# Performance work log

Measured on AMD Instinct MI355X. Metric: run time of the kernel, lower is better.

The kernel has to match this reference:

```python
import jax, jax.numpy as jnp
import numpy as np

N_NODES = 100000
N_EDGES = 1000000
D = 64


def _sage_conv(x_src, x_self, src, dst, W_self, W_neigh, b, n_nodes):
    # mean aggregation over in-neighbors: gather src feats, segment-sum into dst
    gathered = x_src[src]                                            # [E, D]
    summed = jax.ops.segment_sum(gathered, dst, num_segments=n_nodes)  # [N, D]
    deg = jax.ops.segment_sum(jnp.ones_like(dst, dtype=x_src.dtype), dst,
                              num_segments=n_nodes)                  # [N]
    mean = summed / jnp.maximum(deg, 1.0)[:, None]  # zero-degree -> 0 (DGL semantics)
    # DGL SAGEConv: fc_self (with bias) + fc_neigh (no bias)
    return x_self @ W_self + b + mean @ W_neigh


def setup_inputs() -> dict:
    key = jax.random.key(0)
    ks = jax.random.split(key, 8)
    s = 1.0 / np.sqrt(D)
    return {
        "x": jax.random.normal(ks[0], (N_NODES, D), dtype=jnp.float32),
        "src": jax.random.randint(ks[1], (N_EDGES,), 0, N_NODES, dtype=jnp.int32),
        "dst": jax.random.randint(ks[2], (N_EDGES,), 0, N_NODES, dtype=jnp.int32),
        "W_self1": jax.random.normal(ks[3], (D, D), dtype=jnp.float32) * s,
        "W_neigh1": jax.random.normal(ks[4], (D, D), dtype=jnp.float32) * s,
        "b1": jnp.zeros((D,), dtype=jnp.float32),
        "W_self2": jax.random.normal(ks[5], (D, D), dtype=jnp.float32) * s,
        "W_neigh2": jax.random.normal(ks[6], (D, D), dtype=jnp.float32) * s,
        "b2": jnp.zeros((D,), dtype=jnp.float32),
    }


def reference(x, src, dst, W_self1, W_neigh1, b1, W_self2, W_neigh2, b2):
    n = x.shape[0]
    h = _sage_conv(x, x, src, dst, W_self1, W_neigh1, b1, n)
    h = jax.nn.relu(h)
    out = _sage_conv(h, h, src, dst, W_self2, W_neigh2, b2, n)
    return out
```

## Files before the change

### kernel.cpp

```cpp
#include <hip/hip_runtime.h>

#define DFEAT 64
typedef unsigned short bf16_t;

typedef __bf16 bf16x8 __attribute__((ext_vector_type(8)));
typedef float f32x4 __attribute__((ext_vector_type(4)));

#define NPB_SHIFT 7
#define NPB 128
#define BCAP 2048
#define ESLICE 2048
#define MEAN_STRIDE 72

__device__ __forceinline__ float bflo(unsigned int u) {
    union { unsigned int i; float f; } v;
    v.i = u << 16;
    return v.f;
}
__device__ __forceinline__ float bfhi(unsigned int u) {
    union { unsigned int i; float f; } v;
    v.i = u & 0xFFFF0000u;
    return v.f;
}
__device__ __forceinline__ unsigned short f2bf(float f) {
    unsigned int u = __float_as_uint(f);
    u += 0x7FFFu + ((u >> 16) & 1u);
    return (unsigned short)(u >> 16);
}

__global__ __launch_bounds__(256) void prep_all(const int* __restrict__ src,
                                                const int* __restrict__ dst,
                                                int* __restrict__ gcur,
                                                int* __restrict__ packbuf,
                                                int n_edges, int nbuck,
                                                const float* __restrict__ x,
                                                bf16_t* __restrict__ xb,
                                                bf16_t* __restrict__ hb, int n_half,
                                                const float* __restrict__ Ws1,
                                                const float* __restrict__ Wn1,
                                                const float* __restrict__ Ws2,
                                                const float* __restrict__ Wn2,
                                                bf16_t* __restrict__ wf1,
                                                bf16_t* __restrict__ wf2,
                                                int ab, int cb, int n_nodes) {
    const int tid = threadIdx.x;
    const int blk = blockIdx.x;
    if (blk < ab) {
        __shared__ int bhist[1024];
        __shared__ int bcur[1024];
        const long ebase = (long)blk * ESLICE;
        for (int i = tid; i < 1024; i += 256) bhist[i] = 0;
        __syncthreads();
        for (int i = 0; i < ESLICE / 256; ++i) {
            long e = ebase + i * 256 + tid;
            if (e < n_edges) atomicAdd(&bhist[dst[e] >> NPB_SHIFT], 1);
        }
        __syncthreads();
        for (int bb = tid; bb < nbuck; bb += 256) {
            int h = bhist[bb];
            bcur[bb] = h ? atomicAdd(&gcur[bb], h) : 0;
        }
        __syncthreads();
        for (int i = 0; i < ESLICE / 256; ++i) {
            long e = ebase + i * 256 + tid;
            if (e < n_edges) {
                int d = dst[e];
                int bb = d >> NPB_SHIFT;
                int slot = atomicAdd(&bcur[bb], 1);
                if (slot < BCAP)
                    packbuf[(size_t)bb * BCAP + slot] = ((d & (NPB - 1)) << 17) | src[e];
            }
        }
    } else if (blk < ab + cb) {
        int t = (blk - ab) * 256 + tid;
        if (t < n_half) {
            float2 v = ((const float2*)x)[t];
            ushort2 o;
            o.x = f2bf(v.x);
            o.y = f2bf(v.y);
            ((ushort2*)xb)[t] = o;
        }
    } else {
        for (int i = tid; i < 16 * 64 * 8; i += 256) {
            int j = i & 7;
            int l = (i >> 3) & 63;
            int f = i >> 9;
            int kk = f >> 2, nt = f & 3;
            int k = kk * 32 + (l >> 4) * 8 + j;
            int col = nt * 16 + (l & 15);
            float v1 = (k < 64) ? Ws1[k * 64 + col] : Wn1[(k - 64) * 64 + col];
            float v2 = (k < 64) ? Ws2[k * 64 + col] : Wn2[(k - 64) * 64 + col];
            wf1[i] = f2bf(v1);
            wf2[i] = f2bf(v2);
        }
        if (tid < DFEAT) {
            xb[(size_t)n_nodes * DFEAT + tid] = 0;
            hb[(size_t)n_nodes * DFEAT + tid] = 0;
        }
    }
}

__global__ __launch_bounds__(256) void fused_layer(const bf16_t* __restrict__ featb,
                                                   const int* __restrict__ gcur,
                                                   const int* __restrict__ packbuf,
                                                   const bf16_t* __restrict__ wf,
                                                   const float* __restrict__ bias,
                                                   float* __restrict__ outf,
                                                   bf16_t* __restrict__ outb,
                                                   int n_nodes, int do_relu, int zrow) {
    __shared__ int    elist[BCAP];
    __shared__ bf16_t meanL[NPB * MEAN_STRIDE];
    __shared__ int    hist[NPB];
    __shared__ int    scanb[NPB];
    __shared__ int    curL[NPB];

    const int tid = threadIdx.x;
    const int b   = blockIdx.x;

    if (tid < NPB) hist[tid] = 0;
    __syncthreads();

    const int count = min(gcur[b], BCAP);
    const int* pb = packbuf + (size_t)b * BCAP;

    int pkreg[BCAP / 256];
#pragma unroll
    for (int k = 0; k < BCAP / 256; ++k) {
        int i = tid + k * 256;
        if (i < count) {
            int pk = pb[i];
            pkreg[k] = pk;
            atomicAdd(&hist[(pk >> 17) & (NPB - 1)], 1);
        }
    }
    __syncthreads();

    int hv = (tid < NPB) ? hist[tid] : 0;
    int cp = (hv + 3) & ~3;
    if (tid < NPB) scanb[tid] = cp;
    __syncthreads();
    for (int off = 1; off < NPB; off <<= 1) {
        int t = 0;
        if (tid < NPB && tid >= off) t = scanb[tid - off];
        __syncthreads();
        if (tid < NPB) scanb[tid] += t;
        __syncthreads();
    }
    if (tid < NPB) {
        int ex = scanb[tid] - cp;
        scanb[tid] = ex;
        curL[tid]  = ex;
    }
    __syncthreads();

#pragma unroll
    for (int k = 0; k < BCAP / 256; ++k) {
        int i = tid + k * 256;
        if (i < count) {
            int pk = pkreg[k];
            int dl = (pk >> 17) & (NPB - 1);
            int pos = atomicAdd(&curL[dl], 1);
            if (pos < BCAP) elist[pos] = pk & 0x1FFFF;
        }
    }
    __syncthreads();
    if (tid < NPB) {
        int s0 = scanb[tid];
        int c  = hist[tid];
        int ce = s0 + ((c + 3) & ~3);
        for (int p = s0 + c; p < ce && p < BCAP; ++p) elist[p] = zrow;
    }
    __syncthreads();

    const int oct = tid >> 3;
    const int lo  = tid & 7;
#pragma unroll
    for (int n = 0; n < 4; ++n) {
        int r  = oct * 4 + n;
        int s0 = scanb[r];
        int c  = hist[r];
        int cpd = (c + 3) & ~3;
        float s0f = 0.f, s1f = 0.f, s2f = 0.f, s3f = 0.f;
        float s4f = 0.f, s5f = 0.f, s6f = 0.f, s7f = 0.f;
        int i = 0;
        for (; i + 8 <= cpd; i += 8) {
            int4 ea = *(const int4*)(elist + s0 + i);
            int4 eb = *(const int4*)(elist + s0 + i + 4);
            uint4 u0 = *(const uint4*)(featb + (size_t)ea.x * DFEAT + lo * 8);
            uint4 u1 = *(const uint4*)(featb + (size_t)ea.y * DFEAT + lo * 8);
            uint4 u2 = *(const uint4*)(featb + (size_t)ea.z * DFEAT + lo * 8);
            uint4 u3 = *(const uint4*)(featb + (size_t)ea.w * DFEAT + lo * 8);
            uint4 u4 = *(const uint4*)(featb + (size_t)eb.x * DFEAT + lo * 8);
            uint4 u5 = *(const uint4*)(featb + (size_t)eb.y * DFEAT + lo * 8);
            uint4 u6 = *(const uint4*)(featb + (size_t)eb.z * DFEAT + lo * 8);
            uint4 u7 = *(const uint4*)(featb + (size_t)eb.w * DFEAT + lo * 8);
            s0f += bflo(u0.x) + bflo(u1.x) + bflo(u2.x) + bflo(u3.x)
                 + bflo(u4.x) + bflo(u5.x) + bflo(u6.x) + bflo(u7.x);
            s1f += bfhi(u0.x) + bfhi(u1.x) + bfhi(u2.x) + bfhi(u3.x)
                 + bfhi(u4.x) + bfhi(u5.x) + bfhi(u6.x) + bfhi(u7.x);
            s2f += bflo(u0.y) + bflo(u1.y) + bflo(u2.y) + bflo(u3.y)
                 + bflo(u4.y) + bflo(u5.y) + bflo(u6.y) + bflo(u7.y);
            s3f += bfhi(u0.y) + bfhi(u1.y) + bfhi(u2.y) + bfhi(u3.y)
                 + bfhi(u4.y) + bfhi(u5.y) + bfhi(u6.y) + bfhi(u7.y);
            s4f += bflo(u0.z) + bflo(u1.z) + bflo(u2.z) + bflo(u3.z)
                 + bflo(u4.z) + bflo(u5.z) + bflo(u6.z) + bflo(u7.z);
            s5f += bfhi(u0.z) + bfhi(u1.z) + bfhi(u2.z) + bfhi(u3.z)
                 + bfhi(u4.z) + bfhi(u5.z) + bfhi(u6.z) + bfhi(u7.z);
            s6f += bflo(u0.w) + bflo(u1.w) + bflo(u2.w) + bflo(u3.w)
                 + bflo(u4.w) + bflo(u5.w) + bflo(u6.w) + bflo(u7.w);
            s7f += bfhi(u0.w) + bfhi(u1.w) + bfhi(u2.w) + bfhi(u3.w)
                 + bfhi(u4.w) + bfhi(u5.w) + bfhi(u6.w) + bfhi(u7.w);
        }
        if (i < cpd) {
            int4 ea = *(const int4*)(elist + s0 + i);
            uint4 u0 = *(const uint4*)(featb + (size_t)ea.x * DFEAT + lo * 8);
            uint4 u1 = *(const uint4*)(featb + (size_t)ea.y * DFEAT + lo * 8);
            uint4 u2 = *(const uint4*)(featb + (size_t)ea.z * DFEAT + lo * 8);
            uint4 u3 = *(const uint4*)(featb + (size_t)ea.w * DFEAT + lo * 8);
            s0f += bflo(u0.x) + bflo(u1.x) + bflo(u2.x) + bflo(u3.x);
            s1f += bfhi(u0.x) + bfhi(u1.x) + bfhi(u2.x) + bfhi(u3.x);
            s2f += bflo(u0.y) + bflo(u1.y) + bflo(u2.y) + bflo(u3.y);
            s3f += bfhi(u0.y) + bfhi(u1.y) + bfhi(u2.y) + bfhi(u3.y);
            s4f += bflo(u0.z) + bflo(u1.z) + bflo(u2.z) + bflo(u3.z);
            s5f += bfhi(u0.z) + bfhi(u1.z) + bfhi(u2.z) + bfhi(u3.z);
            s6f += bflo(u0.w) + bflo(u1.w) + bflo(u2.w) + bflo(u3.w);
            s7f += bfhi(u0.w) + bfhi(u1.w) + bfhi(u2.w) + bfhi(u3.w);
        }
        float inv = (c > 0) ? 1.0f / (float)c : 0.0f;
        uint4 o;
        o.x = (unsigned int)f2bf(s0f * inv) | ((unsigned int)f2bf(s1f * inv) << 16);
        o.y = (unsigned int)f2bf(s2f * inv) | ((unsigned int)f2bf(s3f * inv) << 16);
        o.z = (unsigned int)f2bf(s4f * inv) | ((unsigned int)f2bf(s5f * inv) << 16);
        o.w = (unsigned int)f2bf(s6f * inv) | ((unsigned int)f2bf(s7f * inv) << 16);
        *(uint4*)(meanL + (size_t)r * MEAN_STRIDE + lo * 8) = o;
    }
    __syncthreads();

    const int lane = tid & 63;
    const int wave = tid >> 6;
    const int q    = lane >> 4;
    const int cgl  = lane & 15;
    const int nodeBase = b << NPB_SHIFT;

    bf16x8 a[2][4];
#pragma unroll
    for (int slab = 0; slab < 2; ++slab) {
        const int r = wave * 32 + slab * 16 + cgl;
        int nodeA = nodeBase + r;
        if (nodeA >= n_nodes) nodeA = n_nodes - 1;
        const bf16_t* xrow = featb + (size_t)nodeA * DFEAT + q * 8;
        a[slab][0] = *(const bf16x8*)(xrow);
        a[slab][1] = *(const bf16x8*)(xrow + 32);
        const bf16_t* mrow = meanL + (size_t)r * MEAN_STRIDE + q * 8;
        a[slab][2] = *(const bf16x8*)(mrow);
        a[slab][3] = *(const bf16x8*)(mrow + 32);
    }

    f32x4 acc[2][4] = {};
#pragma unroll
    for (int nt = 0; nt < 4; ++nt) {
        bf16x8 bf[4];
#pragma unroll
        for (int kk = 0; kk < 4; ++kk)
            bf[kk] = *(const bf16x8*)(wf + (size_t)((kk * 4 + nt) * 64 + lane) * 8);
#pragma unroll
        for (int slab = 0; slab < 2; ++slab) {
#pragma unroll
            for (int kk = 0; kk < 4; ++kk)
                acc[slab][nt] = __builtin_amdgcn_mfma_f32_16x16x32_bf16(
                    a[slab][kk], bf[kk], acc[slab][nt], 0, 0, 0);
        }
    }

#pragma unroll
    for (int slab = 0; slab < 2; ++slab) {
#pragma unroll
        for (int nt = 0; nt < 4; ++nt) {
            const float bl = bias[nt * 16 + cgl];
#pragma unroll
            for (int reg = 0; reg < 4; ++reg) {
                int node = nodeBase + wave * 32 + slab * 16 + q * 4 + reg;
                if (node >= n_nodes) continue;
                float v = acc[slab][nt][reg] + bl;
                if (do_relu) v = fmaxf(v, 0.0f);
                if (outf) outf[(size_t)node * DFEAT + nt * 16 + cgl] = v;
                else      outb[(size_t)node * DFEAT + nt * 16 + cgl] = f2bf(v);
            }
        }
    }
}


extern "C" void kernel_launch(void* const* d_in, const int* in_sizes, int n_in,
                              void* d_out, int out_size, void* d_ws, size_t ws_size,
                              hipStream_t stream) {
    const float* x       = (const float*)d_in[0];
    const int*   src     = (const int*)d_in[1];
    const int*   dst     = (const int*)d_in[2];
    const float* Wself1  = (const float*)d_in[3];
    const float* Wneigh1 = (const float*)d_in[4];
    const float* b1      = (const float*)d_in[5];
    const float* Wself2  = (const float*)d_in[6];
    const float* Wneigh2 = (const float*)d_in[7];
    const float* b2      = (const float*)d_in[8];
    float* out = (float*)d_out;

    int n_nodes = in_sizes[0] / DFEAT;
    int n_edges = in_sizes[1];
    int nbuck   = (n_nodes + NPB - 1) >> NPB_SHIFT;
    int n_half  = n_nodes * DFEAT / 2;

    int* gcur       = (int*)d_ws;
    bf16_t* wf1     = (bf16_t*)(gcur + 1024);
    bf16_t* wf2     = wf1 + 16 * 64 * 8;
    int* packbuf    = (int*)(wf2 + 16 * 64 * 8);
    bf16_t* xb      = (bf16_t*)(packbuf + (size_t)nbuck * BCAP);
    bf16_t* hb      = xb + (size_t)(n_nodes + 1) * DFEAT;

    int ab = (n_edges + ESLICE - 1) / ESLICE;
    int cb = (n_half + 255) / 256;

    hipMemsetAsync(gcur, 0, 1024 * sizeof(int), stream);
    prep_all<<<ab + cb + 1, 256, 0, stream>>>(src, dst, gcur, packbuf,
                                              n_edges, nbuck, x, xb, hb, n_half,
                                              Wself1, Wneigh1, Wself2, Wneigh2,
                                              wf1, wf2, ab, cb, n_nodes);

    fused_layer<<<nbuck, 256, 0, stream>>>(xb, gcur, packbuf, wf1, b1,
                                           nullptr, hb, n_nodes, 1, n_nodes);
    fused_layer<<<nbuck, 256, 0, stream>>>(hb, gcur, packbuf, wf2, b2,
                                           out, nullptr, n_nodes, 0, n_nodes);
}
```

Before: 178.5 us.

## Split each node bucket across two blocks and use wave shuffle scan

Each fused_layer bucket of 128 destination nodes is now handled by two blocks of 64 nodes each. Each block reads the whole packed edge list for its bucket but keeps only the edges whose destination falls in its half. This doubles the grid (about 782 to 1564 blocks) to improve occupancy and latency hiding on the many CUs, and halves shared memory per block. The block-wide LDS scan with repeated barriers is replaced by a single-wave shuffle scan. The cost is that every packed edge entry is read twice, and the MFMA weight fragments are loaded per block with less reuse across slabs.

```diff
diff --git a/kernel.cpp b/kernel.cpp
--- a/kernel.cpp
+++ b/kernel.cpp
@@ -8,7 +8,9 @@
 
 #define NPB_SHIFT 7
 #define NPB 128
+#define HNPB 64
 #define BCAP 2048
+#define ELCAP 1024
 #define ESLICE 2048
 #define MEAN_STRIDE 72
 
@@ -108,46 +110,50 @@
                                                    float* __restrict__ outf,
                                                    bf16_t* __restrict__ outb,
                                                    int n_nodes, int do_relu, int zrow) {
-    __shared__ int    elist[BCAP];
-    __shared__ bf16_t meanL[NPB * MEAN_STRIDE];
-    __shared__ int    hist[NPB];
-    __shared__ int    scanb[NPB];
-    __shared__ int    curL[NPB];
-
-    const int tid = threadIdx.x;
-    const int b   = blockIdx.x;
-
-    if (tid < NPB) hist[tid] = 0;
-    __syncthreads();
-
-    const int count = min(gcur[b], BCAP);
-    const int* pb = packbuf + (size_t)b * BCAP;
+    __shared__ int    elist[ELCAP];
+    __shared__ bf16_t meanL[HNPB * MEAN_STRIDE];
+    __shared__ int    hist[HNPB];
+    __shared__ int    scanb[HNPB];
+    __shared__ int    curL[HNPB];
+
+    const int tid    = threadIdx.x;
+    const int b      = blockIdx.x;
+    const int bucket = b >> 1;
+    const int half   = b & 1;
+
+    if (tid < HNPB) hist[tid] = 0;
+    __syncthreads();
+
+    const int count = min(gcur[bucket], BCAP);
+    const int* pb = packbuf + (size_t)bucket * BCAP;
 
     int pkreg[BCAP / 256];
 #pragma unroll
     for (int k = 0; k < BCAP / 256; ++k) {
         int i = tid + k * 256;
+        int pk = -1;
         if (i < count) {
-            int pk = pb[i];
-            pkreg[k] = pk;
-            atomicAdd(&hist[(pk >> 17) & (NPB - 1)], 1);
-        }
-    }
-    __syncthreads();
-
-    int hv = (tid < NPB) ? hist[tid] : 0;
-    int cp = (hv + 3) & ~3;
-    if (tid < NPB) scanb[tid] = cp;
-    __syncthreads();
-    for (int off = 1; off < NPB; off <<= 1) {
-        int t = 0;
-        if (tid < NPB && tid >= off) t = scanb[tid - off];
-        __syncthreads();
-        if (tid < NPB) scanb[tid] += t;
-        __syncthreads();
-    }
-    if (tid < NPB) {
-        int ex = scanb[tid] - cp;
+            int w = pb[i];
+            int dl = (w >> 17) & (NPB - 1);
+            if ((dl >> 6) == half) {
+                pk = w;
+                atomicAdd(&hist[dl & (HNPB - 1)], 1);
+            }
+        }
+        pkreg[k] = pk;
+    }
+    __syncthreads();
+
+    if (tid < HNPB) {
+        int hv = hist[tid];
+        int v  = (hv + 3) & ~3;
+        int orig = v;
+#pragma unroll
+        for (int off = 1; off < HNPB; off <<= 1) {
+            int u = __shfl_up(v, off, 64);
+            if ((tid & 63) >= off) v += u;
+        }
+        int ex = v - orig;
         scanb[tid] = ex;
         curL[tid]  = ex;
     }
@@ -155,28 +161,27 @@
 
 #pragma unroll
     for (int k = 0; k < BCAP / 256; ++k) {
-        int i = tid + k * 256;
-        if (i < count) {
-            int pk = pkreg[k];
-            int dl = (pk >> 17) & (NPB - 1);
+        int pk = pkreg[k];
+        if (pk >= 0) {
+            int dl = ((pk >> 17) & (NPB - 1)) & (HNPB - 1);
             int pos = atomicAdd(&curL[dl], 1);
-            if (pos < BCAP) elist[pos] = pk & 0x1FFFF;
-        }
-    }
-    __syncthreads();
-    if (tid < NPB) {
+            if (pos < ELCAP) elist[pos] = pk & 0x1FFFF;
+        }
+    }
+    __syncthreads();
+    if (tid < HNPB) {
         int s0 = scanb[tid];
         int c  = hist[tid];
         int ce = s0 + ((c + 3) & ~3);
-        for (int p = s0 + c; p < ce && p < BCAP; ++p) elist[p] = zrow;
+        for (int p = s0 + c; p < ce && p < ELCAP; ++p) elist[p] = zrow;
     }
     __syncthreads();
 
     const int oct = tid >> 3;
     const int lo  = tid & 7;
 #pragma unroll
-    for (int n = 0; n < 4; ++n) {
-        int r  = oct * 4 + n;
+    for (int n = 0; n < 2; ++n) {
+        int r  = oct * 2 + n;
         int s0 = scanb[r];
         int c  = hist[r];
         int cpd = (c + 3) & ~3;
@@ -240,52 +245,43 @@
     const int wave = tid >> 6;
     const int q    = lane >> 4;
     const int cgl  = lane & 15;
-    const int nodeBase = b << NPB_SHIFT;
-
-    bf16x8 a[2][4];
-#pragma unroll
-    for (int slab = 0; slab < 2; ++slab) {
-        const int r = wave * 32 + slab * 16 + cgl;
-        int nodeA = nodeBase + r;
-        if (nodeA >= n_nodes) nodeA = n_nodes - 1;
-        const bf16_t* xrow = featb + (size_t)nodeA * DFEAT + q * 8;
-        a[slab][0] = *(const bf16x8*)(xrow);
-        a[slab][1] = *(const bf16x8*)(xrow + 32);
-        const bf16_t* mrow = meanL + (size_t)r * MEAN_STRIDE + q * 8;
-        a[slab][2] = *(const bf16x8*)(mrow);
-        a[slab][3] = *(const bf16x8*)(mrow + 32);
-    }
-
-    f32x4 acc[2][4] = {};
+    const int nodeBase = b << 6;
+
+    const int r = wave * 16 + cgl;
+    int nodeA = nodeBase + r;
+    if (nodeA >= n_nodes) nodeA = n_nodes - 1;
+    const bf16_t* xrow = featb + (size_t)nodeA * DFEAT + q * 8;
+    bf16x8 a0 = *(const bf16x8*)(xrow);
+    bf16x8 a1 = *(const bf16x8*)(xrow + 32);
+    const bf16_t* mrow = meanL + (size_t)r * MEAN_STRIDE + q * 8;
+    bf16x8 a2 = *(const bf16x8*)(mrow);
+    bf16x8 a3 = *(const bf16x8*)(mrow + 32);
+
+    f32x4 acc[4] = {};
 #pragma unroll
     for (int nt = 0; nt < 4; ++nt) {
-        bf16x8 bf[4];
-#pragma unroll
-        for (int kk = 0; kk < 4; ++kk)
-            bf[kk] = *(const bf16x8*)(wf + (size_t)((kk * 4 + nt) * 64 + lane) * 8);
-#pragma unroll
-        for (int slab = 0; slab < 2; ++slab) {
-#pragma unroll
-            for (int kk = 0; kk < 4; ++kk)
-                acc[slab][nt] = __builtin_amdgcn_mfma_f32_16x16x32_bf16(
-                    a[slab][kk], bf[kk], acc[slab][nt], 0, 0, 0);
-        }
-    }
-
-#pragma unroll
-    for (int slab = 0; slab < 2; ++slab) {
-#pragma unroll
-        for (int nt = 0; nt < 4; ++nt) {
-            const float bl = bias[nt * 16 + cgl];
-#pragma unroll
-            for (int reg = 0; reg < 4; ++reg) {
-                int node = nodeBase + wave * 32 + slab * 16 + q * 4 + reg;
-                if (node >= n_nodes) continue;
-                float v = acc[slab][nt][reg] + bl;
-                if (do_relu) v = fmaxf(v, 0.0f);
-                if (outf) outf[(size_t)node * DFEAT + nt * 16 + cgl] = v;
-                else      outb[(size_t)node * DFEAT + nt * 16 + cgl] = f2bf(v);
-            }
+        const bf16_t* wfb = wf + (size_t)(nt * 64 + lane) * 8;
+        acc[nt] = __builtin_amdgcn_mfma_f32_16x16x32_bf16(
+            a0, *(const bf16x8*)(wfb), acc[nt], 0, 0, 0);
+        acc[nt] = __builtin_amdgcn_mfma_f32_16x16x32_bf16(
+            a1, *(const bf16x8*)(wfb + (size_t)4 * 64 * 8), acc[nt], 0, 0, 0);
+        acc[nt] = __builtin_amdgcn_mfma_f32_16x16x32_bf16(
+            a2, *(const bf16x8*)(wfb + (size_t)8 * 64 * 8), acc[nt], 0, 0, 0);
+        acc[nt] = __builtin_amdgcn_mfma_f32_16x16x32_bf16(
+            a3, *(const bf16x8*)(wfb + (size_t)12 * 64 * 8), acc[nt], 0, 0, 0);
+    }
+
+#pragma unroll
+    for (int nt = 0; nt < 4; ++nt) {
+        const float bl = bias[nt * 16 + cgl];
+#pragma unroll
+        for (int reg = 0; reg < 4; ++reg) {
+            int node = nodeBase + wave * 16 + q * 4 + reg;
+            if (node >= n_nodes) continue;
+            float v = acc[nt][reg] + bl;
+            if (do_relu) v = fmaxf(v, 0.0f);
+            if (outf) outf[(size_t)node * DFEAT + nt * 16 + cgl] = v;
+            else      outb[(size_t)node * DFEAT + nt * 16 + cgl] = f2bf(v);
         }
     }
 }
@@ -319,6 +315,7 @@
 
     int ab = (n_edges + ESLICE - 1) / ESLICE;
     int cb = (n_half + 255) / 256;
+    int fb = nbuck * 2;
 
     hipMemsetAsync(gcur, 0, 1024 * sizeof(int), stream);
     prep_all<<<ab + cb + 1, 256, 0, stream>>>(src, dst, gcur, packbuf,
@@ -326,8 +323,8 @@
                                               Wself1, Wneigh1, Wself2, Wneigh2,
                                               wf1, wf2, ab, cb, n_nodes);
 
-    fused_layer<<<nbuck, 256, 0, stream>>>(xb, gcur, packbuf, wf1, b1,
-                                           nullptr, hb, n_nodes, 1, n_nodes);
-    fused_layer<<<nbuck, 256, 0, stream>>>(hb, gcur, packbuf, wf2, b2,
-                                           out, nullptr, n_nodes, 0, n_nodes);
-}
+    fused_layer<<<fb, 256, 0, stream>>>(xb, gcur, packbuf, wf1, b1,
+                                        nullptr, hb, n_nodes, 1, n_nodes);
+    fused_layer<<<fb, 256, 0, stream>>>(hb, gcur, packbuf, wf2, b2,
+                                        out, nullptr, n_nodes, 0, n_nodes);
+}
```

Result: slower. 184.8 us (+3.5%).
